# Performance work log

Measured on AMD Instinct MI355X. Metric: run time of the kernel, lower is better.

Reference implementation:

```python
import jax, jax.numpy as jnp
import numpy as np

D = 1024
H = 16
HD = D // H
DS = 64
B, L = 2, 2048


def setup_inputs() -> dict:
    key = jax.random.key(0)
    ks = jax.random.split(key, 12)
    s = 0.02
    return {
        "x": jax.random.normal(ks[0], (B, L, D), jnp.float32),
        "subject_embed": jax.random.normal(ks[1], (B, DS), jnp.float32),
        "key_padding_mask": jnp.zeros((B, L), jnp.bool_),
        "Wq": jax.random.normal(ks[2], (D, D), jnp.float32) * s,
        "Wk": jax.random.normal(ks[3], (D, D), jnp.float32) * s,
        "Wv": jax.random.normal(ks[4], (D, D), jnp.float32) * s,
        "Wo": jax.random.normal(ks[5], (D, D), jnp.float32) * s,
        "bo": jnp.zeros((D,), jnp.float32),
        "Wsq": jax.random.normal(ks[6], (DS, D), jnp.float32) * s,
        "bsq": jnp.zeros((D,), jnp.float32),
        "Wsk": jax.random.normal(ks[7], (DS, D), jnp.float32) * s,
        "bsk": jnp.zeros((D,), jnp.float32),
    }


def reference(x, subject_embed, key_padding_mask, Wq, Wk, Wv, Wo, bo, Wsq, bsq, Wsk, bsk):
    scale = 1.0 / jnp.sqrt(jnp.asarray(HD, x.dtype))
    q = x @ Wq + (subject_embed @ Wsq + bsq)[:, None, :]   # [B,L,D]
    k = x @ Wk + (subject_embed @ Wsk + bsk)[:, None, :]
    v = x @ Wv
    # split heads: [B,H,L,hd]
    q = q.reshape(B, L, H, HD).transpose(0, 2, 1, 3)
    k = k.reshape(B, L, H, HD).transpose(0, 2, 1, 3)
    v = v.reshape(B, L, H, HD).transpose(0, 2, 1, 3)
    attn = jnp.einsum('bhqd,bhkd->bhqk', q, k) * scale      # [B,H,L,L]
    attn = jnp.where(key_padding_mask[:, None, None, :], -jnp.inf, attn)
    attn = jax.nn.softmax(attn, axis=-1)
    out = jnp.einsum('bhqk,bhkd->bhqd', attn, v)
    out = out.transpose(0, 2, 1, 3).reshape(B, L, D)
    return out @ Wo + bo
```

## Files before the change

kernel.cpp:

```cpp
#include <hip/hip_runtime.h>
#include <hip/hip_bf16.h>
#include <math.h>

#define DEV __device__ __forceinline__

typedef short bf16x8 __attribute__((ext_vector_type(8)));
typedef short bf16x4 __attribute__((ext_vector_type(4)));
typedef float f32x4 __attribute__((ext_vector_type(4)));

static constexpr int D  = 1024;
static constexpr int H  = 16;
static constexpr int HD = 64;
static constexpr int DS = 64;
static constexpr int B  = 2;
static constexpr int L  = 2048;
static constexpr int M  = B * L;

static constexpr float QSCALE = 0.18033688011112042f;

DEV unsigned short f2bf(float f) {
  union { float f; unsigned u; } x; x.f = f;
  unsigned r = (x.u + 0x7FFFu + ((x.u >> 16) & 1u)) >> 16;
  return (unsigned short)r;
}

DEV unsigned pack2bf(float a, float b) {
  return (unsigned)f2bf(a) | ((unsigned)f2bf(b) << 16);
}

DEV unsigned pack2bf_trunc(float a, float b) {
  union { float f; unsigned u; } ua{a}, ub{b};
  return (ua.u >> 16) | (ub.u & 0xffff0000u);
}

DEV void gload_lds16(const void* g, void* l) {
  __builtin_amdgcn_global_load_lds(
      (const __attribute__((address_space(1))) unsigned int*)g,
      (__attribute__((address_space(3))) unsigned int*)l, 16, 0, 0);
}

__global__ __launch_bounds__(256) void prep_kernel(
    const float* __restrict__ Wq, const float* __restrict__ Wk,
    const float* __restrict__ Wv, const float* __restrict__ Wo,
    const float* __restrict__ x, const float* __restrict__ subj,
    const float* __restrict__ Wsq, const float* __restrict__ bsq,
    const float* __restrict__ Wsk, const float* __restrict__ bsk,
    unsigned short* __restrict__ WT4, unsigned short* __restrict__ xb,
    float* __restrict__ sq, float* __restrict__ sk) {
  __shared__ float tile[64][65];
  const int blk = blockIdx.x, t = threadIdx.x;
  if (blk < 1024) {
    const int z = blk >> 8, idx = blk & 255;
    const float* W = z == 0 ? Wq : z == 1 ? Wk : z == 2 ? Wv : Wo;
    unsigned short* dst = WT4 + (size_t)z * D * D;
    const int n0 = (idx & 15) * 64, k0 = (idx >> 4) * 64;
    const int c = t & 63, r4 = t >> 6;
#pragma unroll
    for (int rr = 0; rr < 16; ++rr) {
      int row = r4 + rr * 4;
      tile[row][c] = W[(size_t)(k0 + row) * D + n0 + c];
    }
    __syncthreads();
#pragma unroll
    for (int rr = 0; rr < 16; ++rr) {
      int nrow = r4 + rr * 4;
      dst[(size_t)(n0 + nrow) * D + k0 + c] = f2bf(tile[c][nrow]);
    }
  } else if (blk < 3072) {
    size_t g = (size_t)(blk - 1024) * 256 + t;
    const float4* xf = (const float4*)x;
    float4 a = xf[2 * g], b = xf[2 * g + 1];
    union { unsigned short s[8]; uint4 v; } o;
    o.s[0] = f2bf(a.x); o.s[1] = f2bf(a.y); o.s[2] = f2bf(a.z); o.s[3] = f2bf(a.w);
    o.s[4] = f2bf(b.x); o.s[5] = f2bf(b.y); o.s[6] = f2bf(b.z); o.s[7] = f2bf(b.w);
    ((uint4*)xb)[g] = o.v;
  } else {
    int g = (blk - 3072) * 256 + t;
    int ty = g >> 11, b = (g >> 10) & 1, n = g & 1023;
    const float* W = ty ? Wsk : Wsq;
    const float* bias = ty ? bsk : bsq;
    float s = bias[n];
#pragma unroll 8
    for (int d = 0; d < DS; ++d) s += subj[b * DS + d] * W[d * D + n];
    (ty ? sk : sq)[b * D + n] = s;
  }
}

__global__ __launch_bounds__(256) void proj_kernel(
    const unsigned short* __restrict__ xb, const unsigned short* __restrict__ WT3,
    const float* __restrict__ sq, const float* __restrict__ sk,
    unsigned short* __restrict__ qk, unsigned short* __restrict__ vT) {
  __shared__ __align__(16) unsigned short smem[128 * 136];
  unsigned short* As = smem;
  unsigned short* Bs = smem + 128 * 64;
  const int z = blockIdx.z;
  const unsigned short* Wt = WT3 + (size_t)z * D * D;
  const int m0 = blockIdx.y * 128, n0 = blockIdx.x * 128;
  const int t = threadIdx.x, l = t & 63, w = t >> 6;
  const int wm = w >> 1, wn = w & 1;
  const int lm = l & 15, lq = l >> 4;
  const int srow8 = t >> 3;
  const int fsw = ((t & 7) ^ ((t >> 3) & 7)) * 8;
  const int swm = lm & 7;
  f32x4 acc[4][4] = {};
  for (int kt = 0; kt < D / 64; ++kt) {
    const int kb = kt * 64;
#pragma unroll
    for (int c = 0; c < 4; ++c) {
      int row = 32 * c + srow8;
      gload_lds16(&xb[(size_t)(m0 + row) * D + kb + fsw], &As[(32 * c + 8 * w) * 64]);
      gload_lds16(&Wt[(size_t)(n0 + row) * D + kb + fsw], &Bs[(32 * c + 8 * w) * 64]);
    }
    __syncthreads();
#pragma unroll
    for (int kk = 0; kk < 2; ++kk) {
      bf16x8 af[4], bf[4];
#pragma unroll
      for (int i = 0; i < 4; ++i)
        af[i] = *(const bf16x8*)&As[(64 * wm + 16 * i + lm) * 64 + ((kk * 4 + lq) ^ swm) * 8];
#pragma unroll
      for (int j = 0; j < 4; ++j)
        bf[j] = *(const bf16x8*)&Bs[(64 * wn + 16 * j + lm) * 64 + ((kk * 4 + lq) ^ swm) * 8];
#pragma unroll
      for (int i = 0; i < 4; ++i)
#pragma unroll
        for (int j = 0; j < 4; ++j)
          acc[i][j] = __builtin_amdgcn_mfma_f32_16x16x32_bf16(af[i], bf[j], acc[i][j], 0, 0, 0);
    }
    __syncthreads();
  }
  if (z == 2) {
#pragma unroll
    for (int i = 0; i < 4; ++i)
#pragma unroll
      for (int j = 0; j < 4; ++j) {
        int cr = 64 * wn + 16 * j + lm;
        int rr = 64 * wm + 16 * i + 4 * lq;
        uint2 u;
        u.x = pack2bf(acc[i][j][0], acc[i][j][1]);
        u.y = pack2bf(acc[i][j][2], acc[i][j][3]);
        *(uint2*)&smem[cr * 136 + rr] = u;
      }
    __syncthreads();
    const int cr = t >> 1, half = t & 1;
    const int bb = m0 >> 11, l0 = m0 & (L - 1);
    const int gcol = n0 + cr, h = gcol >> 6, hd = gcol & 63;
    size_t dbase = ((size_t)(bb * H + h) * HD + hd) * L + l0 + half * 64;
#pragma unroll
    for (int c = 0; c < 8; ++c) {
      uint4 u = *(const uint4*)&smem[cr * 136 + half * 64 + c * 8];
      *(uint4*)&vT[dbase + c * 8] = u;
    }
  } else {
    unsigned short* dst = qk + (size_t)z * M * D;
    const float* bias = z == 0 ? sq : sk;
    const float post = z == 0 ? QSCALE : 1.0f;
#pragma unroll
    for (int i = 0; i < 4; ++i)
#pragma unroll
      for (int j = 0; j < 4; ++j)
#pragma unroll
        for (int r = 0; r < 4; ++r) {
          int rr = 64 * wm + 16 * i + 4 * lq + r;
          int cc = 64 * wn + 16 * j + lm;
          float v = (acc[i][j][r] + bias[((m0 + rr) >> 11) * D + n0 + cc]) * post;
          smem[rr * 136 + cc] = f2bf(v);
        }
    __syncthreads();
    const int row = t >> 1, half = t & 1;
    const int bb = m0 >> 11, ll = (m0 & (L - 1)) + row;
    const int h0 = (n0 >> 6) + half;
    size_t dbase = ((size_t)(bb * H + h0) * L + ll) * HD;
#pragma unroll
    for (int c = 0; c < 8; ++c) {
      uint4 u = *(const uint4*)&smem[row * 136 + half * 64 + c * 8];
      *(uint4*)&dst[dbase + c * 8] = u;
    }
  }
}

__global__ __launch_bounds__(256) void attn_kernel(
    const unsigned short* __restrict__ q_hm, const unsigned short* __restrict__ k_hm,
    const unsigned short* __restrict__ vT, const unsigned char* __restrict__ mask,
    unsigned short* __restrict__ ctx) {
  __shared__ unsigned short Qs[128 * 64];
  __shared__ unsigned short Ksb[2 * 128 * 64];
  __shared__ unsigned short Vtb[2 * 64 * 128];
  const int bx = blockIdx.x;
  const int rest = bx >> 3;
  const int bhid = (bx & 7) + 8 * (rest >> 4);
  const int q0 = (rest & 15) * 128;
  const int h = bhid & 15, b = bhid >> 4;
  const size_t bh = (size_t)(b * H + h);
  const unsigned short* qp = q_hm + bh * L * HD;
  const unsigned short* kp = k_hm + bh * L * HD;
  const unsigned short* vp = vT + bh * HD * L;
  const int t = threadIdx.x, l = t & 63, w = t >> 6;
  const int lm = l & 15, lq = l >> 4;
  const int fsw = ((t & 7) ^ ((t >> 3) & 7)) * 8;
  const int swm = lm & 7;
  const int srow = t >> 3;
  const int vs = t & 15, vr = t >> 4;
  const int vcsrc = ((vs & 8) | ((vs & 7) ^ (vr & 7))) * 8;

#pragma unroll
  for (int c = 0; c < 4; ++c) {
    gload_lds16(&qp[(size_t)(q0 + 32 * c + srow) * HD + fsw], &Qs[(32 * c + 8 * w) * 64]);
    gload_lds16(&kp[(size_t)(32 * c + srow) * HD + fsw], &Ksb[(32 * c + 8 * w) * 64]);
    gload_lds16(&vp[(size_t)(16 * c + vr) * L + vcsrc], &Vtb[(16 * c + 4 * w) * 128]);
  }
  __syncthreads();
  bf16x8 qf[2][2];
#pragma unroll
  for (int i = 0; i < 2; ++i)
#pragma unroll
    for (int kk = 0; kk < 2; ++kk)
      qf[i][kk] = *(const bf16x8*)&Qs[(w * 32 + 16 * i + lm) * 64 + ((kk * 4 + lq) ^ swm) * 8];

  float lsum[2] = {0.f, 0.f};
  f32x4 ot[2][4] = {};

  for (int kt = 0; kt < L / 128; ++kt) {
    const int cur = kt & 1;
    const unsigned short* Kc = Ksb + cur * (128 * 64);
    const unsigned short* Vc = Vtb + cur * (64 * 128);
    unsigned char mby0 = mask[b * L + kt * 128 + l];
    unsigned char mby1 = mask[b * L + kt * 128 + 64 + l];
    if (kt + 1 < L / 128) {
      const int nk0 = (kt + 1) * 128;
      unsigned short* Kd = Ksb + (cur ^ 1) * (128 * 64);
      unsigned short* Vd = Vtb + (cur ^ 1) * (64 * 128);
#pragma unroll
      for (int c = 0; c < 4; ++c) {
        gload_lds16(&kp[(size_t)(nk0 + 32 * c + srow) * HD + fsw], &Kd[(32 * c + 8 * w) * 64]);
        gload_lds16(&vp[(size_t)(16 * c + vr) * L + nk0 + vcsrc], &Vd[(16 * c + 4 * w) * 128]);
      }
    }
    unsigned long long mb0 = __ballot(mby0 != 0);
    unsigned long long mb1 = __ballot(mby1 != 0);

#pragma unroll
    for (int jt = 0; jt < 8; ++jt) {
      bf16x8 kf0 = *(const bf16x8*)&Kc[(16 * jt + lm) * 64 + ((0 + lq) ^ swm) * 8];
      bf16x8 kf1 = *(const bf16x8*)&Kc[(16 * jt + lm) * 64 + ((4 + lq) ^ swm) * 8];
      f32x4 st[2];
#pragma unroll
      for (int i = 0; i < 2; ++i) {
        f32x4 a = {};
        a = __builtin_amdgcn_mfma_f32_16x16x32_bf16(kf0, qf[i][0], a, 0, 0, 0);
        a = __builtin_amdgcn_mfma_f32_16x16x32_bf16(kf1, qf[i][1], a, 0, 0, 0);
        st[i] = a;
      }
      unsigned long long mbX = jt < 4 ? mb0 : mb1;
      if (mbX) {
        int jm = jt & 3;
        unsigned bits = (unsigned)(mbX >> (4 * lq + 16 * jm));
#pragma unroll
        for (int i = 0; i < 2; ++i)
#pragma unroll
          for (int r = 0; r < 4; ++r)
            if ((bits >> r) & 1u) st[i][r] = -1e30f;
      }
      union { uint2 u; bf16x4 v; } pp[2];
#pragma unroll
      for (int i = 0; i < 2; ++i) {
        f32x4 p;
        float ps = 0.f;
#pragma unroll
        for (int r = 0; r < 4; ++r) {
          float e = __builtin_amdgcn_exp2f(st[i][r]);
          p[r] = e;
          ps += e;
        }
        lsum[i] += ps;
        pp[i].u.x = pack2bf_trunc(p[0], p[1]);
        pp[i].u.y = pack2bf_trunc(p[2], p[3]);
      }
      const int kc2 = 2 * jt + (lq >> 1);
      const int slot = (kc2 & 8) | ((kc2 & 7) ^ swm);
#pragma unroll
      for (int jf = 0; jf < 4; ++jf) {
        bf16x4 vb = *(const bf16x4*)&Vc[(16 * jf + lm) * 128 + slot * 8 + 4 * (lq & 1)];
#pragma unroll
        for (int i = 0; i < 2; ++i)
          ot[i][jf] = __builtin_amdgcn_mfma_f32_16x16x16bf16_1k(
              pp[i].v, vb, ot[i][jf], 0, 0, 0);
      }
    }
    __syncthreads();
  }

  float rl[2];
#pragma unroll
  for (int i = 0; i < 2; ++i) {
    float s = lsum[i];
    s += __shfl_xor(s, 16, 64);
    s += __shfl_xor(s, 32, 64);
    rl[i] = 1.0f / s;
  }

  unsigned short* Es = Ksb;
#pragma unroll
  for (int i = 0; i < 2; ++i) {
    float rlq[4];
#pragma unroll
    for (int r = 0; r < 4; ++r) rlq[r] = __shfl(rl[i], 4 * lq + r, 64);
#pragma unroll
    for (int jf = 0; jf < 4; ++jf)
#pragma unroll
      for (int r = 0; r < 4; ++r)
        Es[(w * 32 + 16 * i + 4 * lq + r) * 72 + 16 * jf + lm] =
            f2bf(ot[i][jf][r] * rlq[r]);
  }
  {
    int row = l >> 1, half = l & 1;
    size_t obase = ((size_t)(b * L + q0 + w * 32 + row)) * D + h * HD + half * 32;
#pragma unroll
    for (int c = 0; c < 4; ++c) {
      uint4 u = *(const uint4*)&Es[(w * 32 + row) * 72 + half * 32 + c * 8];
      *(uint4*)&ctx[obase + c * 8] = u;
    }
  }
}

__global__ __launch_bounds__(256) void outgemm_kernel(
    const unsigned short* __restrict__ ctx, const unsigned short* __restrict__ WoT,
    const float* __restrict__ bo, float* __restrict__ out) {
  __shared__ unsigned short As[64 * 64];
  __shared__ unsigned short Bs[128 * 64];
  const int m0 = blockIdx.y * 64, n0 = blockIdx.x * 128;
  const int t = threadIdx.x, l = t & 63, w = t >> 6;
  const int wm = w >> 1, wn = w & 1;
  const int lm = l & 15, lq = l >> 4;
  const int srow8 = t >> 3;
  const int fsw = ((t & 7) ^ ((t >> 3) & 7)) * 8;
  const int swm = lm & 7;
  f32x4 acc[2][4] = {};
  for (int kt = 0; kt < D / 64; ++kt) {
    const int kb = kt * 64;
#pragma unroll
    for (int c = 0; c < 2; ++c)
      gload_lds16(&ctx[(size_t)(m0 + 32 * c + srow8) * D + kb + fsw],
                  &As[(32 * c + 8 * w) * 64]);
#pragma unroll
    for (int c = 0; c < 4; ++c)
      gload_lds16(&WoT[(size_t)(n0 + 32 * c + srow8) * D + kb + fsw],
                  &Bs[(32 * c + 8 * w) * 64]);
    __syncthreads();
#pragma unroll
    for (int kk = 0; kk < 2; ++kk) {
      bf16x8 af[2], bf[4];
#pragma unroll
      for (int i = 0; i < 2; ++i)
        af[i] = *(const bf16x8*)&As[(32 * wm + 16 * i + lm) * 64 + ((kk * 4 + lq) ^ swm) * 8];
#pragma unroll
      for (int j = 0; j < 4; ++j)
        bf[j] = *(const bf16x8*)&Bs[(64 * wn + 16 * j + lm) * 64 + ((kk * 4 + lq) ^ swm) * 8];
#pragma unroll
      for (int i = 0; i < 2; ++i)
#pragma unroll
        for (int j = 0; j < 4; ++j)
          acc[i][j] = __builtin_amdgcn_mfma_f32_16x16x32_bf16(af[i], bf[j], acc[i][j], 0, 0, 0);
    }
    __syncthreads();
  }
#pragma unroll
  for (int i = 0; i < 2; ++i)
#pragma unroll
    for (int j = 0; j < 4; ++j)
#pragma unroll
      for (int r = 0; r < 4; ++r) {
        int grow = m0 + 32 * wm + 16 * i + lq * 4 + r;
        int gcol = n0 + 64 * wn + 16 * j + lm;
        out[(size_t)grow * D + gcol] = acc[i][j][r] + bo[gcol];
      }
}

extern "C" void kernel_launch(void* const* d_in, const int* in_sizes, int n_in,
                              void* d_out, int out_size, void* d_ws, size_t ws_size,
                              hipStream_t stream) {
  const float* x    = (const float*)d_in[0];
  const float* subj = (const float*)d_in[1];
  const unsigned char* mask = (const unsigned char*)d_in[2];
  const float* Wq = (const float*)d_in[3];
  const float* Wk = (const float*)d_in[4];
  const float* Wv = (const float*)d_in[5];
  const float* Wo = (const float*)d_in[6];
  const float* bo = (const float*)d_in[7];
  const float* Wsq = (const float*)d_in[8];
  const float* bsq = (const float*)d_in[9];
  const float* Wsk = (const float*)d_in[10];
  const float* bsk = (const float*)d_in[11];
  float* out = (float*)d_out;
  char* ws = (char*)d_ws;

  unsigned short* xb  = (unsigned short*)(ws);
  unsigned short* WT4 = (unsigned short*)(ws + (8ull  << 20));
  unsigned short* qk  = (unsigned short*)(ws + (16ull << 20));
  unsigned short* ctx = (unsigned short*)(ws + (32ull << 20));
  unsigned short* vT  = (unsigned short*)(ws + (40ull << 20));
  float* sq = (float*)(ws + (48ull << 20));
  float* sk = sq + B * D;

  hipLaunchKernelGGL(prep_kernel, dim3(3088), dim3(256), 0, stream,
                     Wq, Wk, Wv, Wo, x, subj, Wsq, bsq, Wsk, bsk, WT4, xb, sq, sk);
  hipLaunchKernelGGL(proj_kernel, dim3(8, 32, 3), dim3(256), 0, stream,
                     xb, WT4, sq, sk, qk, vT);
  hipLaunchKernelGGL(attn_kernel, dim3(512), dim3(256), 0, stream,
                     qk, qk + (size_t)M * D, vT, mask, ctx);
  hipLaunchKernelGGL(outgemm_kernel, dim3(8, 64, 1), dim3(256), 0, stream, ctx,
                     WT4 + 3ull * D * D, bo, out);
}
```

Before: 216.4 us.

## Split attention key tiles across two wave groups with LDS reduction

The attention kernel goes from 256 to 512 threads per block. Each query wave pair is split so one group handles the first half of each 128-key tile and the other handles the second half. Partial softmax sums and output accumulators are combined through shared memory at the end. This doubles the waves available to hide MFMA and LDS latency per block, at the cost of an extra LDS reduction, a barrier, and higher per-block resource use.

```diff
diff --git a/kernel.cpp b/kernel.cpp
--- a/kernel.cpp
+++ b/kernel.cpp
@@ -179,13 +179,14 @@
   }
 }
 
-__global__ __launch_bounds__(256) void attn_kernel(
+__global__ __launch_bounds__(512, 4) void attn_kernel(
     const unsigned short* __restrict__ q_hm, const unsigned short* __restrict__ k_hm,
     const unsigned short* __restrict__ vT, const unsigned char* __restrict__ mask,
     unsigned short* __restrict__ ctx) {
-  __shared__ unsigned short Qs[128 * 64];
-  __shared__ unsigned short Ksb[2 * 128 * 64];
-  __shared__ unsigned short Vtb[2 * 64 * 128];
+  __shared__ __align__(16) unsigned short smem[40960];
+  unsigned short* Qs  = smem;
+  unsigned short* Ksb = smem + 8192;
+  unsigned short* Vtb = smem + 24576;
   const int bx = blockIdx.x;
   const int rest = bx >> 3;
   const int bhid = (bx & 7) + 8 * (rest >> 4);
@@ -196,6 +197,7 @@
   const unsigned short* kp = k_hm + bh * L * HD;
   const unsigned short* vp = vT + bh * HD * L;
   const int t = threadIdx.x, l = t & 63, w = t >> 6;
+  const int wq = w & 3, wj = w >> 2;
   const int lm = l & 15, lq = l >> 4;
   const int fsw = ((t & 7) ^ ((t >> 3) & 7)) * 8;
   const int swm = lm & 7;
@@ -204,10 +206,10 @@
   const int vcsrc = ((vs & 8) | ((vs & 7) ^ (vr & 7))) * 8;
 
 #pragma unroll
-  for (int c = 0; c < 4; ++c) {
-    gload_lds16(&qp[(size_t)(q0 + 32 * c + srow) * HD + fsw], &Qs[(32 * c + 8 * w) * 64]);
-    gload_lds16(&kp[(size_t)(32 * c + srow) * HD + fsw], &Ksb[(32 * c + 8 * w) * 64]);
-    gload_lds16(&vp[(size_t)(16 * c + vr) * L + vcsrc], &Vtb[(16 * c + 4 * w) * 128]);
+  for (int c = 0; c < 2; ++c) {
+    gload_lds16(&qp[(size_t)(q0 + 64 * c + srow) * HD + fsw], &Qs[(64 * c + 8 * w) * 64]);
+    gload_lds16(&kp[(size_t)(64 * c + srow) * HD + fsw], &Ksb[(64 * c + 8 * w) * 64]);
+    gload_lds16(&vp[(size_t)(32 * c + vr) * L + vcsrc], &Vtb[(32 * c + 4 * w) * 128]);
   }
   __syncthreads();
   bf16x8 qf[2][2];
@@ -215,32 +217,31 @@
   for (int i = 0; i < 2; ++i)
 #pragma unroll
     for (int kk = 0; kk < 2; ++kk)
-      qf[i][kk] = *(const bf16x8*)&Qs[(w * 32 + 16 * i + lm) * 64 + ((kk * 4 + lq) ^ swm) * 8];
+      qf[i][kk] = *(const bf16x8*)&Qs[(wq * 32 + 16 * i + lm) * 64 + ((kk * 4 + lq) ^ swm) * 8];
 
   float lsum[2] = {0.f, 0.f};
   f32x4 ot[2][4] = {};
 
   for (int kt = 0; kt < L / 128; ++kt) {
     const int cur = kt & 1;
-    const unsigned short* Kc = Ksb + cur * (128 * 64);
-    const unsigned short* Vc = Vtb + cur * (64 * 128);
-    unsigned char mby0 = mask[b * L + kt * 128 + l];
-    unsigned char mby1 = mask[b * L + kt * 128 + 64 + l];
+    const unsigned short* Kc = Ksb + cur * 8192;
+    const unsigned short* Vc = Vtb + cur * 8192;
+    unsigned char mby = mask[b * L + kt * 128 + 64 * wj + l];
     if (kt + 1 < L / 128) {
       const int nk0 = (kt + 1) * 128;
-      unsigned short* Kd = Ksb + (cur ^ 1) * (128 * 64);
-      unsigned short* Vd = Vtb + (cur ^ 1) * (64 * 128);
-#pragma unroll
-      for (int c = 0; c < 4; ++c) {
-        gload_lds16(&kp[(size_t)(nk0 + 32 * c + srow) * HD + fsw], &Kd[(32 * c + 8 * w) * 64]);
-        gload_lds16(&vp[(size_t)(16 * c + vr) * L + nk0 + vcsrc], &Vd[(16 * c + 4 * w) * 128]);
-      }
-    }
-    unsigned long long mb0 = __ballot(mby0 != 0);
-    unsigned long long mb1 = __ballot(mby1 != 0);
-
-#pragma unroll
-    for (int jt = 0; jt < 8; ++jt) {
+      unsigned short* Kd = Ksb + (cur ^ 1) * 8192;
+      unsigned short* Vd = Vtb + (cur ^ 1) * 8192;
+#pragma unroll
+      for (int c = 0; c < 2; ++c) {
+        gload_lds16(&kp[(size_t)(nk0 + 64 * c + srow) * HD + fsw], &Kd[(64 * c + 8 * w) * 64]);
+        gload_lds16(&vp[(size_t)(32 * c + vr) * L + nk0 + vcsrc], &Vd[(32 * c + 4 * w) * 128]);
+      }
+    }
+    unsigned long long mb = __ballot(mby != 0);
+
+#pragma unroll
+    for (int jt4 = 0; jt4 < 4; ++jt4) {
+      const int jt = 4 * wj + jt4;
       bf16x8 kf0 = *(const bf16x8*)&Kc[(16 * jt + lm) * 64 + ((0 + lq) ^ swm) * 8];
       bf16x8 kf1 = *(const bf16x8*)&Kc[(16 * jt + lm) * 64 + ((4 + lq) ^ swm) * 8];
       f32x4 st[2];
@@ -251,10 +252,8 @@
         a = __builtin_amdgcn_mfma_f32_16x16x32_bf16(kf1, qf[i][1], a, 0, 0, 0);
         st[i] = a;
       }
-      unsigned long long mbX = jt < 4 ? mb0 : mb1;
-      if (mbX) {
-        int jm = jt & 3;
-        unsigned bits = (unsigned)(mbX >> (4 * lq + 16 * jm));
+      if (mb) {
+        unsigned bits = (unsigned)(mb >> (4 * lq + 16 * jt4));
 #pragma unroll
         for (int i = 0; i < 2; ++i)
 #pragma unroll
@@ -290,34 +289,56 @@
     __syncthreads();
   }
 
-  float rl[2];
+  float* Obuf = (float*)smem;
+  unsigned short* Es = smem + 20480;
+  float* Sred = (float*)(smem + 35840);
+
+  float sums[2];
 #pragma unroll
   for (int i = 0; i < 2; ++i) {
     float s = lsum[i];
     s += __shfl_xor(s, 16, 64);
     s += __shfl_xor(s, 32, 64);
-    rl[i] = 1.0f / s;
-  }
-
-  unsigned short* Es = Ksb;
-#pragma unroll
-  for (int i = 0; i < 2; ++i) {
-    float rlq[4];
-#pragma unroll
-    for (int r = 0; r < 4; ++r) rlq[r] = __shfl(rl[i], 4 * lq + r, 64);
-#pragma unroll
-    for (int jf = 0; jf < 4; ++jf)
-#pragma unroll
-      for (int r = 0; r < 4; ++r)
-        Es[(w * 32 + 16 * i + 4 * lq + r) * 72 + 16 * jf + lm] =
-            f2bf(ot[i][jf][r] * rlq[r]);
-  }
-  {
+    sums[i] = s;
+    Sred[w * 32 + i * 16 + lm] = s;
+  }
+  if (wj) {
+#pragma unroll
+    for (int i = 0; i < 2; ++i)
+#pragma unroll
+      for (int jf = 0; jf < 4; ++jf)
+        *(f32x4*)&Obuf[(16 * jf + lm) * 132 + wq * 32 + 16 * i + 4 * lq] = ot[i][jf];
+  }
+  __syncthreads();
+  if (!wj) {
+    float rl[2];
+#pragma unroll
+    for (int i = 0; i < 2; ++i)
+      rl[i] = 1.0f / (sums[i] + Sred[(w + 4) * 32 + i * 16 + lm]);
+#pragma unroll
+    for (int i = 0; i < 2; ++i)
+#pragma unroll
+      for (int jf = 0; jf < 4; ++jf) {
+        f32x4 po = *(const f32x4*)&Obuf[(16 * jf + lm) * 132 + wq * 32 + 16 * i + 4 * lq];
+        ot[i][jf] += po;
+      }
+#pragma unroll
+    for (int i = 0; i < 2; ++i) {
+      float rlq[4];
+#pragma unroll
+      for (int r = 0; r < 4; ++r) rlq[r] = __shfl(rl[i], 4 * lq + r, 64);
+#pragma unroll
+      for (int jf = 0; jf < 4; ++jf)
+#pragma unroll
+        for (int r = 0; r < 4; ++r)
+          Es[(wq * 32 + 16 * i + 4 * lq + r) * 72 + 16 * jf + lm] =
+              f2bf(ot[i][jf][r] * rlq[r]);
+    }
     int row = l >> 1, half = l & 1;
-    size_t obase = ((size_t)(b * L + q0 + w * 32 + row)) * D + h * HD + half * 32;
+    size_t obase = ((size_t)(b * L + q0 + wq * 32 + row)) * D + h * HD + half * 32;
 #pragma unroll
     for (int c = 0; c < 4; ++c) {
-      uint4 u = *(const uint4*)&Es[(w * 32 + row) * 72 + half * 32 + c * 8];
+      uint4 u = *(const uint4*)&Es[(wq * 32 + row) * 72 + half * 32 + c * 8];
       *(uint4*)&ctx[obase + c * 8] = u;
     }
   }
@@ -406,7 +427,7 @@
                      Wq, Wk, Wv, Wo, x, subj, Wsq, bsq, Wsk, bsk, WT4, xb, sq, sk);
   hipLaunchKernelGGL(proj_kernel, dim3(8, 32, 3), dim3(256), 0, stream,
                      xb, WT4, sq, sk, qk, vT);
-  hipLaunchKernelGGL(attn_kernel, dim3(512), dim3(256), 0, stream,
+  hipLaunchKernelGGL(attn_kernel, dim3(512), dim3(512), 0, stream,
                      qk, qk + (size_t)M * D, vT, mask, ctx);
   hipLaunchKernelGGL(outgemm_kernel, dim3(8, 64, 1), dim3(256), 0, stream, ctx,
                      WT4 + 3ull * D * D, bo, out);
```

Measured after the change: 207.1 us. 4.3% less time.
